# Kernel tuning notes

Hardware: AMD Instinct MI355X
Metric: run time of the kernel (lower is better)

Reference implementation:

```python
import jax, jax.numpy as jnp
import numpy as np

SIGNAL_SIZE = 33554432  # 2**25
N_ELEMENTS = 25         # log2(SIGNAL_SIZE)


def fft_shift(a, shift):
    # Faithful port of the torch fft_shift (note: 'shift' variable is reused
    # in the original; the phase ramp overwrites it after shift_samples).
    shift = 1.0 - shift
    n_samples = a.shape[-1]
    shift_samples = shift * n_samples * 0.5
    spec = jnp.fft.rfft(a, norm='ortho')
    n_coeffs = spec.shape[-1]
    phase = jnp.arange(n_coeffs) * (2j * np.pi / n_coeffs)  # complex64 ramp
    spec = spec * jnp.exp(phase * shift_samples)
    return jnp.fft.irfft(spec, n=n_samples, norm='ortho')


def setup_inputs() -> dict:
    key = jax.random.key(0)
    elements = jax.random.uniform(key, (N_ELEMENTS,), minval=-1.0, maxval=1.0,
                                  dtype=jnp.float32)
    return {"elements": elements}


def reference(elements):
    # dirac impulse of size 2 at position 0
    signal = jnp.zeros(2, dtype=jnp.float32).at[0].set(1.0)
    for i in range(N_ELEMENTS):  # fixed trip count; sizes double each step
        if i > 0:
            new_signal = jnp.zeros(signal.shape[-1] * 2, dtype=signal.dtype)
            signal = new_signal.at[::2].set(signal)
        shift_factor = 1.0 / (2 ** i)
        signal = fft_shift(signal, elements[i] * shift_factor)
    return signal  # shape [SIGNAL_SIZE]
```

## Files before the change

kernel.cpp:

```cpp
#include <hip/hip_runtime.h>


constexpr float PI_F    = 3.14159265358979323846f;
constexpr float TWOPI_F = 6.28318530717958647692f;
constexpr unsigned M24 = 1u << 24;

__device__ __forceinline__ void phase_sincos(float th, float* sn, float* cs) {
    double d = (double)th * 0.15915494309189533577;
    d -= rint(d);
    float ang = (float)(d * 6.2831853071795864769);
    __sincosf(ang, sn, cs);
}

__global__ __launch_bounds__(256) void build_q(const float* __restrict__ el,
                                               float2* __restrict__ Q) {
    __shared__ float c_s[18], s_s[18], T_s[18];
    int tid = threadIdx.x;
    if (tid < 18) {
        float e = el[tid];
        float shift1 = e * (1.0f / (float)(1u << tid));
        float sh2 = 1.0f - shift1;
        float s = sh2 * (float)(1u << tid);
        float c = (float)(6.2831853071795864769 / (double)((1u << tid) + 1u));
        c_s[tid] = c;
        s_s[tid] = s;
        float p  = (float)(1u << tid) * c;
        float th = p * s;
        float sn, cs; phase_sincos(th, &sn, &cs);
        T_s[tid] = cs;
    }
    __syncthreads();

    unsigned r = blockIdx.x * 256u + (unsigned)tid;
    if (r == 0u) { Q[0] = make_float2(1.0f, 0.0f); return; }

    unsigned t = (unsigned)__builtin_ctz(r);
    float Pr = T_s[t], Pi = 0.0f;

#pragma unroll
    for (int i = 1; i <= 17; ++i) {
        unsigned hi = 1u << i;
        int sd = (int)((r + hi) & (2u * hi - 1u)) - (int)hi;
        int K  = (i <= (int)t) ? 0 : (sd < 0 ? -sd : sd);
        float sgn = (sd < 0) ? -1.0f : 1.0f;
        float p  = (float)K * c_s[i];
        float th = p * s_s[i];
        float sn, cs; phase_sincos(th, &sn, &cs);
        float ssn = sgn * sn;
        float nr = Pr * cs - Pi * ssn;
        float ni = Pr * ssn + Pi * cs;
        Pr = nr; Pi = ni;
    }
    Q[r] = make_float2(Pr, Pi);
}

__global__ __launch_bounds__(256) void build_w(const float* __restrict__ el,
                                               const float2* __restrict__ Q,
                                               float2* __restrict__ W) {
    __shared__ float c_s[25], s_s[25], T_s[24];
    int tid = threadIdx.x;
    if (tid < 25) {
        float e = el[tid];
        float shift1 = e * (1.0f / (float)(1u << tid));
        float sh2 = 1.0f - shift1;
        float s = sh2 * (float)(1u << tid);
        float c = (float)(6.2831853071795864769 / (double)((1u << tid) + 1u));
        c_s[tid] = c;
        s_s[tid] = s;
        if (tid < 24) {
            float p  = (float)(1u << tid) * c;
            float th = p * s;
            float sn, cs; phase_sincos(th, &sn, &cs);
            T_s[tid] = cs;
        }
    }
    __syncthreads();

    unsigned k = blockIdx.x * 256u + (unsigned)tid;
    if (k > 8388608u) return;

    const float sc = 1.0f / 33554432.0f;

    if (k == 0u) {
        float p  = 16777216.0f * c_s[24];
        float th = p * s_s[24];
        float sn, cs; phase_sincos(th, &sn, &cs);
        float Smr = cs;
        W[0] = make_float2((1.0f + Smr) * sc, (1.0f - Smr) * sc);
        return;
    }

    unsigned t = (unsigned)__builtin_ctz(k);
    unsigned r = k & 0x3FFFFu;
    float Pr, Pi;
    if (r != 0u) {
        float2 q = Q[r];
        Pr = q.x; Pi = q.y;
    } else {
        Pr = T_s[t]; Pi = 0.0f;
    }

#pragma unroll
    for (int i = 18; i <= 23; ++i) {
        unsigned hi = 1u << i;
        int sd = (int)((k + hi) & (2u * hi - 1u)) - (int)hi;
        int K  = (i <= (int)t) ? 0 : (sd < 0 ? -sd : sd);
        float sgn = (sd < 0) ? -1.0f : 1.0f;
        float p  = (float)K * c_s[i];
        float th = p * s_s[i];
        float sn, cs; phase_sincos(th, &sn, &cs);
        float ssn = sgn * sn;
        float nr = Pr * cs - Pi * ssn;
        float ni = Pr * ssn + Pi * cs;
        Pr = nr; Pi = ni;
    }

    unsigned mk = M24 - k;
    float thk = ((float)k  * c_s[24]) * s_s[24];
    float thm = ((float)mk * c_s[24]) * s_s[24];
    float snk, csk, snm, csm;
    phase_sincos(thk, &snk, &csk);
    phase_sincos(thm, &snm, &csm);

    float Skr = Pr * csk - Pi * snk;
    float Ski = Pr * snk + Pi * csk;
    float Smr = Pr * csm + Pi * snm;
    float Smi = Pr * snm - Pi * csm;

    float Ar = Skr + Smr, Ai = Ski - Smi;
    float Br = Skr - Smr, Bi = Ski + Smi;
    float ang = (float)k * (TWOPI_F / 33554432.0f);
    float ts, tc; __sincosf(ang, &ts, &tc);
    float Cr = tc * Br - ts * Bi;
    float Ci = ts * Br + tc * Bi;

    W[k] = make_float2((Ar - Ci) * sc, (Ai + Cr) * sc);
    if (k != 8388608u)
        W[mk] = make_float2((Ar + Ci) * sc, (Cr - Ai) * sc);
}

__device__ __forceinline__ void bf4(float2* __restrict__ row, int e0, int d,
                                    float2 tw, float2 tw2) {
    float2 x0 = row[e0], x1 = row[e0 + d], x2 = row[e0 + 2*d], x3 = row[e0 + 3*d];
    float2 a0 = make_float2(x0.x + x2.x, x0.y + x2.y);
    float2 d0 = make_float2(x0.x - x2.x, x0.y - x2.y);
    float2 a1 = make_float2(x1.x + x3.x, x1.y + x3.y);
    float2 d1 = make_float2(x1.x - x3.x, x1.y - x3.y);
    float2 a2 = make_float2(d0.x * tw.x - d0.y * tw.y,  d0.x * tw.y + d0.y * tw.x);
    float2 a3 = make_float2(-d1.x * tw.y - d1.y * tw.x, d1.x * tw.x - d1.y * tw.y);
    row[e0]       = make_float2(a0.x + a1.x, a0.y + a1.y);
    float2 u1 = make_float2(a0.x - a1.x, a0.y - a1.y);
    row[e0 + d]   = make_float2(u1.x * tw2.x - u1.y * tw2.y, u1.x * tw2.y + u1.y * tw2.x);
    row[e0 + 2*d] = make_float2(a2.x + a3.x, a2.y + a3.y);
    float2 u3 = make_float2(a2.x - a3.x, a2.y - a3.y);
    row[e0 + 3*d] = make_float2(u3.x * tw2.x - u3.y * tw2.y, u3.x * tw2.y + u3.y * tw2.x);
}

__device__ __forceinline__ void fft256x16_inv(float2 (*lds)[257], int tid) {
    {
        int j2 = tid & 63;
        float s, c; __sincosf((PI_F / 128.0f) * (float)j2, &s, &c);
        float2 tw  = make_float2(c, s);
        float2 tw2 = make_float2(c * c - s * s, 2.0f * c * s);
        __syncthreads();
#pragma unroll
        for (int v = 0; v < 4; ++v) {
            int row = (tid >> 6) + 4 * v;
            bf4(lds[row], j2, 64, tw, tw2);
        }
    }
    {
        int rowb = tid & 15;
        int j2   = tid >> 4;
        float s, c; __sincosf((PI_F / 32.0f) * (float)j2, &s, &c);
        float2 tw  = make_float2(c, s);
        float2 tw2 = make_float2(c * c - s * s, 2.0f * c * s);
        __syncthreads();
#pragma unroll
        for (int v = 0; v < 4; ++v) {
            bf4(lds[rowb], 64 * v + j2, 16, tw, tw2);
        }
    }
    {
        int rowb = tid & 15;
        int j2   = tid >> 6;
        int bbl  = (tid >> 4) & 3;
        float s, c; __sincosf((PI_F / 8.0f) * (float)j2, &s, &c);
        float2 tw  = make_float2(c, s);
        float2 tw2 = make_float2(c * c - s * s, 2.0f * c * s);
        __syncthreads();
#pragma unroll
        for (int v = 0; v < 4; ++v) {
            int bb = bbl + 4 * v;
            bf4(lds[rowb], 16 * bb + j2, 4, tw, tw2);
        }
    }
    {
        int rowb = tid & 15;
        int bbl  = tid >> 4;
        __syncthreads();
#pragma unroll
        for (int v = 0; v < 4; ++v) {
            int e0 = 4 * (bbl + 16 * v);
            float2* row = lds[rowb];
            float2 x0 = row[e0], x1 = row[e0 + 1], x2 = row[e0 + 2], x3 = row[e0 + 3];
            float2 a0 = make_float2(x0.x + x2.x, x0.y + x2.y);
            float2 d0 = make_float2(x0.x - x2.x, x0.y - x2.y);
            float2 a1 = make_float2(x1.x + x3.x, x1.y + x3.y);
            float2 d1 = make_float2(x1.x - x3.x, x1.y - x3.y);
            row[e0]     = make_float2(a0.x + a1.x, a0.y + a1.y);
            row[e0 + 1] = make_float2(a0.x - a1.x, a0.y - a1.y);
            row[e0 + 2] = make_float2(d0.x - d1.y, d0.y + d1.x);
            row[e0 + 3] = make_float2(d0.x + d1.y, d0.y - d1.x);
        }
    }
    __syncthreads();
}

__global__ __launch_bounds__(256) void fft_stage_a(const float2* __restrict__ in,
                                                   float2* __restrict__ out) {
    __shared__ float2 lds[16][257];
    int tid   = threadIdx.x;
    int cbase = blockIdx.x * 16;
#pragma unroll
    for (int u = 0; u < 16; ++u) {
        int e = tid + 256 * u;
        int row = e & 15, k3 = e >> 4;
        lds[row][k3] = in[cbase + row + (k3 << 16)];
    }
    fft256x16_inv(lds, tid);
#pragma unroll
    for (int u = 0; u < 16; ++u) {
        int e = tid + 256 * u;
        int row = e & 15, p = e >> 4;
        int t3 = (int)(__brev((unsigned)p) >> 24);
        out[cbase + row + (t3 << 16)] = lds[row][p];
    }
}

__global__ __launch_bounds__(256) void fft_stage_b(const float2* __restrict__ in,
                                                   float2* __restrict__ out) {
    __shared__ float2 lds[16][257];
    int tid = threadIdx.x;
    int wg  = blockIdx.x;
    int k1b = (wg & 15) * 16;
    int t3  = wg >> 4;
    const float tsc = TWOPI_F / 65536.0f;

    {
        int row = tid & 15;
        int k20 = tid >> 4;
        float sb, cb; __sincosf(tsc * (float)(t3 * k20), &sb, &cb);
        float ss, cs; __sincosf(tsc * (float)(t3 * 16), &ss, &cs);
        float2 w = make_float2(cb, sb);
#pragma unroll
        for (int u = 0; u < 16; ++u) {
            int k2 = k20 + 16 * u;
            float2 v = in[k1b + row + (k2 << 8) + (t3 << 16)];
            lds[row][k2] = make_float2(v.x * w.x - v.y * w.y, v.x * w.y + v.y * w.x);
            float nx = w.x * cs - w.y * ss;
            float ny = w.x * ss + w.y * cs;
            w = make_float2(nx, ny);
        }
    }
    fft256x16_inv(lds, tid);
#pragma unroll
    for (int u = 0; u < 16; ++u) {
        int e = tid + 256 * u;
        int row = e & 15, p = e >> 4;
        int t2 = (int)(__brev((unsigned)p) >> 24);
        out[k1b + row + (t2 << 8) + (t3 << 16)] = lds[row][p];
    }
}

__global__ __launch_bounds__(256) void fft_stage_c(const float2* __restrict__ in,
                                                   float2* __restrict__ out) {
    __shared__ float2 lds[16][257];
    int tid = threadIdx.x;
    int wg  = blockIdx.x;
    int t3b = (wg & 15) * 16;
    int t2  = wg >> 4;
    const float tsc = TWOPI_F / 16777216.0f;

    {
        int k1 = tid;
        int base = (t3b + (t2 << 8)) * k1;
        float sb, cb; __sincosf(tsc * (float)base, &sb, &cb);
        float ss, cs; __sincosf(tsc * (float)k1, &ss, &cs);
        float2 w = make_float2(cb, sb);
#pragma unroll
        for (int u = 0; u < 16; ++u) {
            float2 v = in[k1 + (t2 << 8) + ((t3b + u) << 16)];
            lds[u][k1] = make_float2(v.x * w.x - v.y * w.y, v.x * w.y + v.y * w.x);
            float nx = w.x * cs - w.y * ss;
            float ny = w.x * ss + w.y * cs;
            w = make_float2(nx, ny);
        }
    }
    fft256x16_inv(lds, tid);
#pragma unroll
    for (int u = 0; u < 16; ++u) {
        int e = tid + 256 * u;
        int r = e & 15, p = e >> 4;
        int t1 = (int)(__brev((unsigned)p) >> 24);
        out[(t3b + r) + (t2 << 8) + (t1 << 16)] = lds[r][p];
    }
}

extern "C" void kernel_launch(void* const* d_in, const int* in_sizes, int n_in,
                              void* d_out, int out_size, void* d_ws, size_t ws_size,
                              hipStream_t stream) {
    const float* el = (const float*)d_in[0];
    float2* W  = (float2*)d_ws;
    float2* Gd = (float2*)d_out;
    float2* Q  = (float2*)d_out;

    hipLaunchKernelGGL(build_q,     dim3(1024),  dim3(256), 0, stream, el, Q);
    hipLaunchKernelGGL(build_w,     dim3(32769), dim3(256), 0, stream, el, Q, W);
    hipLaunchKernelGGL(fft_stage_a, dim3(4096),  dim3(256), 0, stream, W, Gd);
    hipLaunchKernelGGL(fft_stage_b, dim3(4096),  dim3(256), 0, stream, Gd, W);
    hipLaunchKernelGGL(fft_stage_c, dim3(4096),  dim3(256), 0, stream, W, Gd);
}
```

Before: 295.4 us.

## Fuse spectrum-building into the first FFT stage to remove the intermediate buffer

The build_w kernel and fft_stage_a are merged into one kernel that computes the spectrum coefficients directly into shared memory before running the first 256-point inverse FFT pass. Each block is assigned a set of column indices (c_of_row) so that every coefficient k and its mirror M24-k land in the same block, which keeps the pairwise construction. This removes one full write and one full read of the 2^25-element complex intermediate in global memory. In exchange the compute-heavy sincos chain now runs inside the FFT kernel, which may lower occupancy; the index mapping and the special cases for block 0 add complexity. Q moves to the workspace buffer, which is only overwritten later by stage b.

```diff
diff --git a/kernel.cpp b/kernel.cpp
--- a/kernel.cpp
+++ b/kernel.cpp
@@ -54,9 +54,155 @@
     Q[r] = make_float2(Pr, Pi);
 }
 
-__global__ __launch_bounds__(256) void build_w(const float* __restrict__ el,
-                                               const float2* __restrict__ Q,
-                                               float2* __restrict__ W) {
+struct WPair { float2 wk, wmk; };
+
+__device__ __forceinline__ WPair chain_W(unsigned k,
+                                         const float* __restrict__ c_s,
+                                         const float* __restrict__ s_s,
+                                         const float* __restrict__ T_s,
+                                         const float2* __restrict__ Q) {
+    const float sc = 1.0f / 33554432.0f;
+    unsigned t = (unsigned)__builtin_ctz(k);
+    unsigned r = k & 0x3FFFFu;
+    float Pr, Pi;
+    if (r != 0u) {
+        float2 q = Q[r];
+        Pr = q.x; Pi = q.y;
+    } else {
+        Pr = T_s[t]; Pi = 0.0f;
+    }
+
+#pragma unroll
+    for (int i = 18; i <= 23; ++i) {
+        unsigned hi = 1u << i;
+        int sd = (int)((k + hi) & (2u * hi - 1u)) - (int)hi;
+        int K  = (i <= (int)t) ? 0 : (sd < 0 ? -sd : sd);
+        float sgn = (sd < 0) ? -1.0f : 1.0f;
+        float p  = (float)K * c_s[i];
+        float th = p * s_s[i];
+        float sn, cs; phase_sincos(th, &sn, &cs);
+        float ssn = sgn * sn;
+        float nr = Pr * cs - Pi * ssn;
+        float ni = Pr * ssn + Pi * cs;
+        Pr = nr; Pi = ni;
+    }
+
+    unsigned mk = M24 - k;
+    float thk = ((float)k  * c_s[24]) * s_s[24];
+    float thm = ((float)mk * c_s[24]) * s_s[24];
+    float snk, csk, snm, csm;
+    phase_sincos(thk, &snk, &csk);
+    phase_sincos(thm, &snm, &csm);
+
+    float Skr = Pr * csk - Pi * snk;
+    float Ski = Pr * snk + Pi * csk;
+    float Smr = Pr * csm + Pi * snm;
+    float Smi = Pr * snm - Pi * csm;
+
+    float Ar = Skr + Smr, Ai = Ski - Smi;
+    float Br = Skr - Smr, Bi = Ski + Smi;
+    float ang = (float)k * (TWOPI_F / 33554432.0f);
+    float ts, tc; __sincosf(ang, &ts, &tc);
+    float Cr = tc * Br - ts * Bi;
+    float Ci = ts * Br + tc * Bi;
+
+    WPair w;
+    w.wk  = make_float2((Ar - Ci) * sc, (Ai + Cr) * sc);
+    w.wmk = make_float2((Ar + Ci) * sc, (Cr - Ai) * sc);
+    return w;
+}
+
+__device__ __forceinline__ void bf4(float2* __restrict__ row, int e0, int d,
+                                    float2 tw, float2 tw2) {
+    float2 x0 = row[e0], x1 = row[e0 + d], x2 = row[e0 + 2*d], x3 = row[e0 + 3*d];
+    float2 a0 = make_float2(x0.x + x2.x, x0.y + x2.y);
+    float2 d0 = make_float2(x0.x - x2.x, x0.y - x2.y);
+    float2 a1 = make_float2(x1.x + x3.x, x1.y + x3.y);
+    float2 d1 = make_float2(x1.x - x3.x, x1.y - x3.y);
+    float2 a2 = make_float2(d0.x * tw.x - d0.y * tw.y,  d0.x * tw.y + d0.y * tw.x);
+    float2 a3 = make_float2(-d1.x * tw.y - d1.y * tw.x, d1.x * tw.x - d1.y * tw.y);
+    row[e0]       = make_float2(a0.x + a1.x, a0.y + a1.y);
+    float2 u1 = make_float2(a0.x - a1.x, a0.y - a1.y);
+    row[e0 + d]   = make_float2(u1.x * tw2.x - u1.y * tw2.y, u1.x * tw2.y + u1.y * tw2.x);
+    row[e0 + 2*d] = make_float2(a2.x + a3.x, a2.y + a3.y);
+    float2 u3 = make_float2(a2.x - a3.x, a2.y - a3.y);
+    row[e0 + 3*d] = make_float2(u3.x * tw2.x - u3.y * tw2.y, u3.x * tw2.y + u3.y * tw2.x);
+}
+
+__device__ __forceinline__ void fft256x16_inv(float2 (*lds)[257], int tid) {
+    {
+        int j2 = tid & 63;
+        float s, c; __sincosf((PI_F / 128.0f) * (float)j2, &s, &c);
+        float2 tw  = make_float2(c, s);
+        float2 tw2 = make_float2(c * c - s * s, 2.0f * c * s);
+        __syncthreads();
+#pragma unroll
+        for (int v = 0; v < 4; ++v) {
+            int row = (tid >> 6) + 4 * v;
+            bf4(lds[row], j2, 64, tw, tw2);
+        }
+    }
+    {
+        int rowb = tid & 15;
+        int j2   = tid >> 4;
+        float s, c; __sincosf((PI_F / 32.0f) * (float)j2, &s, &c);
+        float2 tw  = make_float2(c, s);
+        float2 tw2 = make_float2(c * c - s * s, 2.0f * c * s);
+        __syncthreads();
+#pragma unroll
+        for (int v = 0; v < 4; ++v) {
+            bf4(lds[rowb], 64 * v + j2, 16, tw, tw2);
+        }
+    }
+    {
+        int rowb = tid & 15;
+        int j2   = tid >> 6;
+        int bbl  = (tid >> 4) & 3;
+        float s, c; __sincosf((PI_F / 8.0f) * (float)j2, &s, &c);
+        float2 tw  = make_float2(c, s);
+        float2 tw2 = make_float2(c * c - s * s, 2.0f * c * s);
+        __syncthreads();
+#pragma unroll
+        for (int v = 0; v < 4; ++v) {
+            int bb = bbl + 4 * v;
+            bf4(lds[rowb], 16 * bb + j2, 4, tw, tw2);
+        }
+    }
+    {
+        int rowb = tid & 15;
+        int bbl  = tid >> 4;
+        __syncthreads();
+#pragma unroll
+        for (int v = 0; v < 4; ++v) {
+            int e0 = 4 * (bbl + 16 * v);
+            float2* row = lds[rowb];
+            float2 x0 = row[e0], x1 = row[e0 + 1], x2 = row[e0 + 2], x3 = row[e0 + 3];
+            float2 a0 = make_float2(x0.x + x2.x, x0.y + x2.y);
+            float2 d0 = make_float2(x0.x - x2.x, x0.y - x2.y);
+            float2 a1 = make_float2(x1.x + x3.x, x1.y + x3.y);
+            float2 d1 = make_float2(x1.x - x3.x, x1.y - x3.y);
+            row[e0]     = make_float2(a0.x + a1.x, a0.y + a1.y);
+            row[e0 + 1] = make_float2(a0.x - a1.x, a0.y - a1.y);
+            row[e0 + 2] = make_float2(d0.x - d1.y, d0.y + d1.x);
+            row[e0 + 3] = make_float2(d0.x + d1.y, d0.y - d1.x);
+        }
+    }
+    __syncthreads();
+}
+
+__device__ __forceinline__ int c_of_row(int b, int r) {
+    if (b == 0) {
+        if (r < 8)  return r;
+        if (r == 8) return 32768;
+        return 65536 - (r - 8);
+    }
+    return (r < 8) ? (8 * b + r) : (65536 - 8 * b - (r - 8));
+}
+
+__global__ __launch_bounds__(256, 4) void fused_build_fft_a(const float* __restrict__ el,
+                                                            const float2* __restrict__ Q,
+                                                            float2* __restrict__ out) {
+    __shared__ float2 lds[16][257];
     __shared__ float c_s[25], s_s[25], T_s[24];
     int tid = threadIdx.x;
     if (tid < 25) {
@@ -76,165 +222,41 @@
     }
     __syncthreads();
 
-    unsigned k = blockIdx.x * 256u + (unsigned)tid;
-    if (k > 8388608u) return;
-
-    const float sc = 1.0f / 33554432.0f;
-
-    if (k == 0u) {
-        float p  = 16777216.0f * c_s[24];
-        float th = p * s_s[24];
-        float sn, cs; phase_sincos(th, &sn, &cs);
-        float Smr = cs;
-        W[0] = make_float2((1.0f + Smr) * sc, (1.0f - Smr) * sc);
-        return;
-    }
-
-    unsigned t = (unsigned)__builtin_ctz(k);
-    unsigned r = k & 0x3FFFFu;
-    float Pr, Pi;
-    if (r != 0u) {
-        float2 q = Q[r];
-        Pr = q.x; Pi = q.y;
-    } else {
-        Pr = T_s[t]; Pi = 0.0f;
-    }
-
-#pragma unroll
-    for (int i = 18; i <= 23; ++i) {
-        unsigned hi = 1u << i;
-        int sd = (int)((k + hi) & (2u * hi - 1u)) - (int)hi;
-        int K  = (i <= (int)t) ? 0 : (sd < 0 ? -sd : sd);
-        float sgn = (sd < 0) ? -1.0f : 1.0f;
-        float p  = (float)K * c_s[i];
-        float th = p * s_s[i];
-        float sn, cs; phase_sincos(th, &sn, &cs);
-        float ssn = sgn * sn;
-        float nr = Pr * cs - Pi * ssn;
-        float ni = Pr * ssn + Pi * cs;
-        Pr = nr; Pi = ni;
-    }
-
-    unsigned mk = M24 - k;
-    float thk = ((float)k  * c_s[24]) * s_s[24];
-    float thm = ((float)mk * c_s[24]) * s_s[24];
-    float snk, csk, snm, csm;
-    phase_sincos(thk, &snk, &csk);
-    phase_sincos(thm, &snm, &csm);
-
-    float Skr = Pr * csk - Pi * snk;
-    float Ski = Pr * snk + Pi * csk;
-    float Smr = Pr * csm + Pi * snm;
-    float Smi = Pr * snm - Pi * csm;
-
-    float Ar = Skr + Smr, Ai = Ski - Smi;
-    float Br = Skr - Smr, Bi = Ski + Smi;
-    float ang = (float)k * (TWOPI_F / 33554432.0f);
-    float ts, tc; __sincosf(ang, &ts, &tc);
-    float Cr = tc * Br - ts * Bi;
-    float Ci = ts * Br + tc * Bi;
-
-    W[k] = make_float2((Ar - Ci) * sc, (Ai + Cr) * sc);
-    if (k != 8388608u)
-        W[mk] = make_float2((Ar + Ci) * sc, (Cr - Ai) * sc);
-}
-
-__device__ __forceinline__ void bf4(float2* __restrict__ row, int e0, int d,
-                                    float2 tw, float2 tw2) {
-    float2 x0 = row[e0], x1 = row[e0 + d], x2 = row[e0 + 2*d], x3 = row[e0 + 3*d];
-    float2 a0 = make_float2(x0.x + x2.x, x0.y + x2.y);
-    float2 d0 = make_float2(x0.x - x2.x, x0.y - x2.y);
-    float2 a1 = make_float2(x1.x + x3.x, x1.y + x3.y);
-    float2 d1 = make_float2(x1.x - x3.x, x1.y - x3.y);
-    float2 a2 = make_float2(d0.x * tw.x - d0.y * tw.y,  d0.x * tw.y + d0.y * tw.x);
-    float2 a3 = make_float2(-d1.x * tw.y - d1.y * tw.x, d1.x * tw.x - d1.y * tw.y);
-    row[e0]       = make_float2(a0.x + a1.x, a0.y + a1.y);
-    float2 u1 = make_float2(a0.x - a1.x, a0.y - a1.y);
-    row[e0 + d]   = make_float2(u1.x * tw2.x - u1.y * tw2.y, u1.x * tw2.y + u1.y * tw2.x);
-    row[e0 + 2*d] = make_float2(a2.x + a3.x, a2.y + a3.y);
-    float2 u3 = make_float2(a2.x - a3.x, a2.y - a3.y);
-    row[e0 + 3*d] = make_float2(u3.x * tw2.x - u3.y * tw2.y, u3.x * tw2.y + u3.y * tw2.x);
-}
-
-__device__ __forceinline__ void fft256x16_inv(float2 (*lds)[257], int tid) {
-    {
-        int j2 = tid & 63;
-        float s, c; __sincosf((PI_F / 128.0f) * (float)j2, &s, &c);
-        float2 tw  = make_float2(c, s);
-        float2 tw2 = make_float2(c * c - s * s, 2.0f * c * s);
-        __syncthreads();
-#pragma unroll
-        for (int v = 0; v < 4; ++v) {
-            int row = (tid >> 6) + 4 * v;
-            bf4(lds[row], j2, 64, tw, tw2);
-        }
-    }
-    {
-        int rowb = tid & 15;
-        int j2   = tid >> 4;
-        float s, c; __sincosf((PI_F / 32.0f) * (float)j2, &s, &c);
-        float2 tw  = make_float2(c, s);
-        float2 tw2 = make_float2(c * c - s * s, 2.0f * c * s);
-        __syncthreads();
-#pragma unroll
-        for (int v = 0; v < 4; ++v) {
-            bf4(lds[rowb], 64 * v + j2, 16, tw, tw2);
-        }
-    }
-    {
-        int rowb = tid & 15;
-        int j2   = tid >> 6;
-        int bbl  = (tid >> 4) & 3;
-        float s, c; __sincosf((PI_F / 8.0f) * (float)j2, &s, &c);
-        float2 tw  = make_float2(c, s);
-        float2 tw2 = make_float2(c * c - s * s, 2.0f * c * s);
-        __syncthreads();
-#pragma unroll
-        for (int v = 0; v < 4; ++v) {
-            int bb = bbl + 4 * v;
-            bf4(lds[rowb], 16 * bb + j2, 4, tw, tw2);
-        }
-    }
-    {
-        int rowb = tid & 15;
-        int bbl  = tid >> 4;
-        __syncthreads();
-#pragma unroll
-        for (int v = 0; v < 4; ++v) {
-            int e0 = 4 * (bbl + 16 * v);
-            float2* row = lds[rowb];
-            float2 x0 = row[e0], x1 = row[e0 + 1], x2 = row[e0 + 2], x3 = row[e0 + 3];
-            float2 a0 = make_float2(x0.x + x2.x, x0.y + x2.y);
-            float2 d0 = make_float2(x0.x - x2.x, x0.y - x2.y);
-            float2 a1 = make_float2(x1.x + x3.x, x1.y + x3.y);
-            float2 d1 = make_float2(x1.x - x3.x, x1.y - x3.y);
-            row[e0]     = make_float2(a0.x + a1.x, a0.y + a1.y);
-            row[e0 + 1] = make_float2(a0.x - a1.x, a0.y - a1.y);
-            row[e0 + 2] = make_float2(d0.x - d1.y, d0.y + d1.x);
-            row[e0 + 3] = make_float2(d0.x + d1.y, d0.y - d1.x);
-        }
-    }
-    __syncthreads();
-}
-
-__global__ __launch_bounds__(256) void fft_stage_a(const float2* __restrict__ in,
-                                                   float2* __restrict__ out) {
-    __shared__ float2 lds[16][257];
-    int tid   = threadIdx.x;
-    int cbase = blockIdx.x * 16;
-#pragma unroll
-    for (int u = 0; u < 16; ++u) {
-        int e = tid + 256 * u;
-        int row = e & 15, k3 = e >> 4;
-        lds[row][k3] = in[cbase + row + (k3 << 16)];
-    }
+    int b   = blockIdx.x;
+    int r   = tid & 15;
+    int k30 = tid >> 4;
+    int c   = c_of_row(b, r);
+    int rm  = (b == 0 && (r == 0 || r == 8)) ? r : (r ^ 8);
+
+#pragma unroll 1
+    for (int u = 0; u < 8; ++u) {
+        int k3 = k30 + 16 * u;
+        unsigned j = (unsigned)c + ((unsigned)k3 << 16);
+        if (b == 0 && r == 0 && k3 == 0) {
+            float p  = 16777216.0f * c_s[24];
+            float th = p * s_s[24];
+            float sn, cs; phase_sincos(th, &sn, &cs);
+            const float sc = 1.0f / 33554432.0f;
+            lds[0][0] = make_float2((1.0f + cs) * sc, (1.0f - cs) * sc);
+            WPair w = chain_W(8388608u, c_s, s_s, T_s, Q);
+            lds[0][128] = w.wk;
+        } else {
+            WPair w = chain_W(j, c_s, s_s, T_s, Q);
+            lds[r][k3] = w.wk;
+            int k3m = (b == 0 && r == 0) ? (256 - k3) : (255 - k3);
+            lds[rm][k3m] = w.wmk;
+        }
+    }
+
     fft256x16_inv(lds, tid);
+
 #pragma unroll
     for (int u = 0; u < 16; ++u) {
         int e = tid + 256 * u;
         int row = e & 15, p = e >> 4;
         int t3 = (int)(__brev((unsigned)p) >> 24);
-        out[cbase + row + (t3 << 16)] = lds[row][p];
+        int cr = c_of_row(b, row);
+        out[cr + (t3 << 16)] = lds[row][p];
     }
 }
 
@@ -246,7 +268,6 @@
     int k1b = (wg & 15) * 16;
     int t3  = wg >> 4;
     const float tsc = TWOPI_F / 65536.0f;
-
     {
         int row = tid & 15;
         int k20 = tid >> 4;
@@ -281,7 +302,6 @@
     int t3b = (wg & 15) * 16;
     int t2  = wg >> 4;
     const float tsc = TWOPI_F / 16777216.0f;
-
     {
         int k1 = tid;
         int base = (t3b + (t2 << 8)) * k1;
@@ -311,13 +331,11 @@
                               void* d_out, int out_size, void* d_ws, size_t ws_size,
                               hipStream_t stream) {
     const float* el = (const float*)d_in[0];
-    float2* W  = (float2*)d_ws;
     float2* Gd = (float2*)d_out;
-    float2* Q  = (float2*)d_out;
-
-    hipLaunchKernelGGL(build_q,     dim3(1024),  dim3(256), 0, stream, el, Q);
-    hipLaunchKernelGGL(build_w,     dim3(32769), dim3(256), 0, stream, el, Q, W);
-    hipLaunchKernelGGL(fft_stage_a, dim3(4096),  dim3(256), 0, stream, W, Gd);
-    hipLaunchKernelGGL(fft_stage_b, dim3(4096),  dim3(256), 0, stream, Gd, W);
-    hipLaunchKernelGGL(fft_stage_c, dim3(4096),  dim3(256), 0, stream, W, Gd);
-}
+    float2* Q  = (float2*)d_ws;
+
+    hipLaunchKernelGGL(build_q,          dim3(1024), dim3(256), 0, stream, el, Q);
+    hipLaunchKernelGGL(fused_build_fft_a, dim3(4096), dim3(256), 0, stream, el, Q, Gd);
+    hipLaunchKernelGGL(fft_stage_b,      dim3(4096), dim3(256), 0, stream, Gd, (float2*)d_ws);
+    hipLaunchKernelGGL(fft_stage_c,      dim3(4096), dim3(256), 0, stream, (float2*)d_ws, Gd);
+}
```

New measurement: 288.5 us. 2.4% less time.
